# Optimization experiments

Measured on AMD Instinct MI355X. Metric: run time of the kernel, lower is better.

The kernel has to match this reference:

```python
import jax, jax.numpy as jnp
import numpy as np

EPS = 1e-5
B, CIN, COUT, H, W, RED = 2, 64, 128, 256, 256, 8
K = 9  # 3x3 deformable kernel taps


def conv2d(x, w, b=None, pad=0):
    out = jax.lax.conv_general_dilated(x, w, (1, 1), [(pad, pad), (pad, pad)],
                                       dimension_numbers=('NCHW', 'OIHW', 'NCHW'))
    return out if b is None else out + b[None, :, None, None]


def batchnorm(x, g, b, m, v):
    s = g / jnp.sqrt(v + EPS)
    return x * s[None, :, None, None] + (b - m * s)[None, :, None, None]


def bilinear_sample(x, py, px):
    # x:(B,C,H,W), py/px:(B,K,H,W) float coords -> (B,C,K,H,W); zero outside bounds
    Bx, C, Hx, Wx = x.shape
    y0 = jnp.floor(py); x0 = jnp.floor(px)
    flat = x.reshape(Bx, C, Hx * Wx)

    def gather(yi, xi):
        valid = (yi >= 0) & (yi < Hx) & (xi >= 0) & (xi < Wx)
        idx = jnp.clip(yi, 0, Hx - 1) * Wx + jnp.clip(xi, 0, Wx - 1)
        g = jax.vmap(lambda f, i: jnp.take(f, i, axis=1))(flat, idx.reshape(Bx, -1))
        return g.reshape(Bx, C, *yi.shape[1:]) * valid[:, None].astype(x.dtype)

    wy1 = (py - y0)[:, None]; wy0 = 1.0 - wy1
    wx1 = (px - x0)[:, None]; wx0 = 1.0 - wx1
    y0i = y0.astype(jnp.int32); x0i = x0.astype(jnp.int32)
    return (gather(y0i, x0i) * wy0 * wx0 + gather(y0i, x0i + 1) * wy0 * wx1 +
            gather(y0i + 1, x0i) * wy1 * wx0 + gather(y0i + 1, x0i + 1) * wy1 * wx1)


def deform_conv(x, offsets, w, b):
    # torchvision DeformConv2d v1: offsets (B, 2*K, H, W), (dy,dx) per tap, row-major taps
    Bx, Cin, Hx, Wx = x.shape
    off = offsets.reshape(Bx, K, 2, Hx, Wx)
    ky, kx = jnp.meshgrid(jnp.arange(3), jnp.arange(3), indexing='ij')
    base_y = (jnp.arange(Hx)[None, :, None] + (ky.reshape(K) - 1)[:, None, None]).astype(x.dtype)  # (K,H,1)
    base_x = (jnp.arange(Wx)[None, None, :] + (kx.reshape(K) - 1)[:, None, None]).astype(x.dtype)  # (K,1,W)
    py = base_y[None] + off[:, :, 0]  # (B,K,H,W)
    px = base_x[None] + off[:, :, 1]
    sampled = bilinear_sample(x, py, px)  # (B,Cin,K,H,W)
    out = jnp.einsum('bckhw,ock->bohw', sampled, w.reshape(w.shape[0], Cin, K))
    return out + b[None, :, None, None]


def setup_inputs() -> dict:
    key = jax.random.key(0)
    ks = jax.random.split(key, 20)
    r = lambda i, shape, s=1.0: jax.random.normal(ks[i], shape, jnp.float32) * s
    cr = COUT // RED
    return dict(
        x=r(0, (B, CIN, H, W)),
        w_off=r(1, (2 * K, CIN, 3, 3), 0.04), b_off=jnp.zeros((2 * K,), jnp.float32),
        w_def=r(2, (COUT, CIN, 3, 3), 0.04), b_def=r(3, (COUT,), 0.01),
        bn_gamma=jnp.ones((COUT,), jnp.float32) + r(4, (COUT,), 0.1),
        bn_beta=r(5, (COUT,), 0.1),
        bn_mean=r(6, (COUT,), 0.1),
        bn_var=jax.random.uniform(ks[7], (COUT,), jnp.float32, 0.5, 1.5),
        se_w=r(8, (cr, COUT, 1, 1), 0.1), se_b=r(9, (cr,), 0.01),
        se_bn_gamma=jnp.ones((cr,), jnp.float32) + r(10, (cr,), 0.1),
        se_bn_beta=r(11, (cr,), 0.1),
        se_bn_mean=r(12, (cr,), 0.1),
        se_bn_var=jax.random.uniform(ks[13], (cr,), jnp.float32, 0.5, 1.5),
        phi=r(14, (cr, COUT), 0.3),
        ds_w=r(15, (COUT, CIN, 1, 1), 0.1),
        ds_bn_gamma=jnp.ones((COUT,), jnp.float32) + r(16, (COUT,), 0.1),
        ds_bn_beta=r(17, (COUT,), 0.1),
        ds_bn_mean=r(18, (COUT,), 0.1),
        ds_bn_var=jax.random.uniform(ks[19], (COUT,), jnp.float32, 0.5, 1.5),
    )


def reference(x, w_off, b_off, w_def, b_def, bn_gamma, bn_beta, bn_mean, bn_var,
              se_w, se_b, se_bn_gamma, se_bn_beta, se_bn_mean, se_bn_var, phi,
              ds_w, ds_bn_gamma, ds_bn_beta, ds_bn_mean, ds_bn_var):
    offsets = conv2d(x, w_off, b_off, pad=1)
    out = deform_conv(x, offsets, w_def, b_def)
    out = batchnorm(out, bn_gamma, bn_beta, bn_mean, bn_var)
    # DCSE: global-avg-pool -> 1x1 conv -> BN -> GELU -> matmul with softmax(phi) -> sigmoid gate
    pooled = out.mean(axis=(2, 3))  # (B,COUT)
    t = pooled @ se_w[:, :, 0, 0].T + se_b  # (B,COUT//RED)
    s = se_bn_gamma / jnp.sqrt(se_bn_var + EPS)
    t = jax.nn.gelu(t * s[None] + (se_bn_beta - se_bn_mean * s)[None], approximate=False)
    dw = jax.nn.sigmoid(t @ jax.nn.softmax(phi, axis=-1))  # (B,COUT)
    out = out * dw[:, :, None, None]
    identity = batchnorm(conv2d(x, ds_w), ds_bn_gamma, ds_bn_beta, ds_bn_mean, ds_bn_var)
    return jax.nn.relu(out + identity)
```

## Files before the change

### kernel.cpp

```cpp
#include <hip/hip_runtime.h>
#include <hip/hip_bf16.h>

typedef __hip_bfloat16 bf16;
typedef unsigned int u32;
typedef __attribute__((ext_vector_type(8))) short bf16x8;
typedef __attribute__((ext_vector_type(4))) float f32x4;

#define HHW 65536
#define SBH 584
#define SWU 292
#define REDW 132

__device__ __forceinline__ float b2f(bf16 v) { return __bfloat162float(v); }
__device__ __forceinline__ bf16  f2b(float v) { return __float2bfloat16(v); }
__device__ __forceinline__ float blo(u32 p) { return __uint_as_float(p << 16); }
__device__ __forceinline__ float bhi(u32 p) { return __uint_as_float(p & 0xffff0000u); }
__device__ __forceinline__ u32 pack2(float lo, float hi) {
    bf16 a = f2b(lo), c = f2b(hi);
    unsigned short ua, uc;
    __builtin_memcpy(&ua, &a, 2); __builtin_memcpy(&uc, &c, 2);
    return (u32)ua | ((u32)uc << 16);
}

__global__ __launch_bounds__(256) void k_prep(const float* __restrict__ x, bf16* __restrict__ xT,
        const float* __restrict__ w_off, const float* __restrict__ w_def, const float* __restrict__ b_def,
        const float* __restrict__ bng, const float* __restrict__ bnb, const float* __restrict__ bnm, const float* __restrict__ bnv,
        const float* __restrict__ ds_w, const float* __restrict__ dsg, const float* __restrict__ dsb,
        const float* __restrict__ dsm, const float* __restrict__ dsv,
        bf16* __restrict__ Wf, float* __restrict__ wloff, float* __restrict__ dws2,
        float* __restrict__ bnS, float* __restrict__ bnT2, float* __restrict__ dsT) {
    __shared__ bf16 tile[64][66];
    int g = blockIdx.x;
    int t = threadIdx.x;
    if (g < 2048) {
        int b = g >> 10;
        int pixbase = (g & 1023) << 6;
        int pix = t & 63, ci0 = t >> 6;
        const float* xb = x + ((size_t)b * 64) * HHW + pixbase + pix;
        for (int ci = ci0; ci < 64; ci += 4)
            tile[pix][ci] = f2b(xb[(size_t)ci * HHW]);
        __syncthreads();
        bf16* dst = xT + ((size_t)b * HHW + pixbase) * 64;
        for (int i = t; i < 4096; i += 256)
            dst[i] = tile[i >> 6][i & 63];
        return;
    }
    int tid = (g - 2048) * 256 + t;
    for (int i = tid; i < 8 * 18 * 64 * 8; i += 8192) {
        int j = i & 7, lane = (i >> 3) & 63;
        int rem = i >> 9;
        int ks = rem % 18, ct = rem / 18;
        int co = ct * 16 + (lane & 15);
        int K  = ks * 32 + ((lane >> 4) << 3) + j;
        int ci = K & 63, kk = K >> 6;
        Wf[i] = f2b(w_def[co * 576 + ci * 9 + kk]);
    }
    for (int i = tid; i < 576 * 20; i += 8192) {
        int kci = i / 20, j = i - kci * 20;
        wloff[i] = (j < 18) ? w_off[j * 576 + kci] : 0.f;
    }
    if (tid < 8192) {
        int co = tid >> 6;
        float s2 = dsg[co] * rsqrtf(dsv[co] + 1e-5f);
        dws2[tid] = ds_w[tid] * s2;
    }
    if (tid < 128) {
        float s = bng[tid] * rsqrtf(bnv[tid] + 1e-5f);
        bnS[tid] = s;
        bnT2[tid] = (b_def[tid] - bnm[tid]) * s + bnb[tid];
        float s2 = dsg[tid] * rsqrtf(dsv[tid] + 1e-5f);
        dsT[tid] = dsb[tid] - dsm[tid] * s2;
    }
}

__global__ __launch_bounds__(256) void k_off(const float* __restrict__ x,
        const float* __restrict__ wloff, const float* __restrict__ b_off,
        uint4* __restrict__ orec, float4* __restrict__ wrec) {
    int g = blockIdx.x;
    int b = g >> 8, h = g & 255;
    int t = threadIdx.x;
    float acc[20];
    #pragma unroll
    for (int j = 0; j < 20; ++j) acc[j] = 0.f;
    const float* xb = x + ((size_t)b * 64) * HHW;
    for (int ci = 0; ci < 64; ++ci) {
        const float* xc = xb + (size_t)ci * HHW;
        #pragma unroll
        for (int ky = 0; ky < 3; ++ky) {
            int y = h + ky - 1;
            if ((unsigned)y >= 256u) continue;
            const float* row = xc + y * 256;
            float v0 = (t >= 1)   ? row[t - 1] : 0.f;
            float v1 = row[t];
            float v2 = (t <= 254) ? row[t + 1] : 0.f;
            const float4* wr = (const float4*)(wloff + (ci * 9 + ky * 3) * 20);
            #pragma unroll
            for (int q = 0; q < 5; ++q) {
                float4 wv = wr[q];
                acc[q*4+0] += v0 * wv.x; acc[q*4+1] += v0 * wv.y;
                acc[q*4+2] += v0 * wv.z; acc[q*4+3] += v0 * wv.w;
            }
            #pragma unroll
            for (int q = 0; q < 5; ++q) {
                float4 wv = wr[5 + q];
                acc[q*4+0] += v1 * wv.x; acc[q*4+1] += v1 * wv.y;
                acc[q*4+2] += v1 * wv.z; acc[q*4+3] += v1 * wv.w;
            }
            #pragma unroll
            for (int q = 0; q < 5; ++q) {
                float4 wv = wr[10 + q];
                acc[q*4+0] += v2 * wv.x; acc[q*4+1] += v2 * wv.y;
                acc[q*4+2] += v2 * wv.z; acc[q*4+3] += v2 * wv.w;
            }
        }
    }
    int tile = (h << 2) + (t >> 6);
    int pix  = t & 63;
    size_t rbase = ((size_t)(b * 1024 + tile)) * 576;
    #pragma unroll
    for (int k = 0; k < 9; ++k) {
        int ky = k / 3, kx = k - ky * 3;
        float dy = acc[2 * k]     + b_off[2 * k];
        float dx = acc[2 * k + 1] + b_off[2 * k + 1];
        float py = (float)(h + ky - 1) + dy;
        float px = (float)(t + kx - 1) + dx;
        float fy = floorf(py), fx = floorf(px);
        int y0 = (int)fy, x0 = (int)fx;
        float wy1 = py - fy, wx1 = px - fx;
        float wy0 = 1.f - wy1, wx0 = 1.f - wx1;
        int y1 = y0 + 1, x1 = x0 + 1;
        int yc0 = min(max(y0, 0), 255), yc1 = min(max(y1, 0), 255);
        int xc0 = min(max(x0, 0), 255), xc1 = min(max(x1, 0), 255);
        float m0 = ((unsigned)y0 < 256u) ? 1.f : 0.f;
        float m1 = ((unsigned)y1 < 256u) ? 1.f : 0.f;
        float n0 = ((unsigned)x0 < 256u) ? 1.f : 0.f;
        float n1 = ((unsigned)x1 < 256u) ? 1.f : 0.f;
        uint4 o;
        o.x = ((u32)(yc0 * 256 + xc0)) << 5;
        o.y = ((u32)(yc0 * 256 + xc1)) << 5;
        o.z = ((u32)(yc1 * 256 + xc0)) << 5;
        o.w = ((u32)(yc1 * 256 + xc1)) << 5;
        float4 wv;
        wv.x = wy0 * wx0 * m0 * n0;
        wv.y = wy0 * wx1 * m0 * n1;
        wv.z = wy1 * wx0 * m1 * n0;
        wv.w = wy1 * wx1 * m1 * n1;
        orec[rbase + k * 64 + pix] = o;
        wrec[rbase + k * 64 + pix] = wv;
    }
}

__global__ __launch_bounds__(256) void k_deform(const bf16* __restrict__ xT,
        const uint4* __restrict__ orec, const float4* __restrict__ wrec,
        const bf16* __restrict__ Wf,
        const float* __restrict__ bnS, const float* __restrict__ bnT2,
        bf16* __restrict__ out_pre, float* __restrict__ part) {
    __shared__ bf16 smem[64 * SBH];
    int blk = blockIdx.x;
    int b = blk >> 10;
    int tile = blk & 1023;
    int pixbase = tile << 6;
    int t = threadIdx.x;
    int wid = t >> 6, l = t & 63;

    {
        int cig = l & 31, hf = l >> 5;
        size_t rbase = ((size_t)(b * 1024 + tile)) * 576;
        const uint4*  orc = orec + rbase;
        const float4* wrc = wrec + rbase;
        const u32* xw = (const u32*)xT + (size_t)b * (HHW * 32);
        u32* sw = (u32*)smem;
        #pragma unroll 4
        for (int it = 0; it < 72; ++it) {
            int r = (it << 3) + (wid << 1) + hf;
            uint4  o  = orc[r];
            float4 wv = wrc[r];
            u32 p00 = xw[o.x + cig];
            u32 p01 = xw[o.y + cig];
            u32 p10 = xw[o.z + cig];
            u32 p11 = xw[o.w + cig];
            float lo = blo(p00)*wv.x + blo(p01)*wv.y + blo(p10)*wv.z + blo(p11)*wv.w;
            float hi = bhi(p00)*wv.x + bhi(p01)*wv.y + bhi(p10)*wv.z + bhi(p11)*wv.w;
            int k9 = r >> 6, pix = r & 63;
            sw[pix * SWU + (k9 << 5) + cig] = pack2(lo, hi);
        }
    }
    __syncthreads();

    int wp = wid << 4;
    int lr = l & 15, lg = l >> 4;
    f32x4 acc[8];
    #pragma unroll
    for (int ct = 0; ct < 8; ++ct) acc[ct] = (f32x4){0.f, 0.f, 0.f, 0.f};
    const bf16* arow = smem + (wp + lr) * SBH + lg * 8;
    const bf16* wbase = Wf + l * 8;
    #pragma unroll
    for (int ks = 0; ks < 18; ++ks) {
        bf16x8 af = *(const bf16x8*)(arow + ks * 32);
        #pragma unroll
        for (int ct = 0; ct < 8; ++ct) {
            bf16x8 bfr = *(const bf16x8*)(wbase + (ct * 18 + ks) * 512);
            acc[ct] = __builtin_amdgcn_mfma_f32_16x16x32_bf16(af, bfr, acc[ct], 0, 0, 0);
        }
    }
    __syncthreads();
    float* red = (float*)smem;
    #pragma unroll
    for (int ct = 0; ct < 8; ++ct) {
        int co = ct * 16 + lr;
        float sc = bnS[co], sh = bnT2[co];
        #pragma unroll
        for (int r = 0; r < 4; ++r) {
            int m = lg * 4 + r;
            red[(wp + m) * REDW + co] = acc[ct][r] * sc + sh;
        }
    }
    __syncthreads();
    bf16* op = out_pre + ((size_t)b * HHW + pixbase) * 128;
    for (int i = t; i < 8192; i += 256)
        op[i] = f2b(red[(i >> 7) * REDW + (i & 127)]);
    if (t < 128) {
        float sum = 0.f;
        #pragma unroll
        for (int p = 0; p < 64; ++p) sum += red[p * REDW + t];
        part[((size_t)(b * 128 + t)) * 1024 + tile] = sum;
    }
}

__global__ __launch_bounds__(256) void k_pool(const float* __restrict__ part, float* __restrict__ pooled) {
    int bco = blockIdx.x;
    int t = threadIdx.x;
    const float* p = part + (size_t)bco * 1024;
    float sum = 0.f;
    for (int i = t; i < 1024; i += 256) sum += p[i];
    __shared__ float r[256];
    r[t] = sum; __syncthreads();
    for (int ofs = 128; ofs > 0; ofs >>= 1) {
        if (t < ofs) r[t] += r[t + ofs];
        __syncthreads();
    }
    if (t == 0) pooled[bco] = r[0] * (1.f / 65536.f);
}

__global__ __launch_bounds__(256) void k_se(const float* __restrict__ pooled,
        const float* __restrict__ se_w, const float* __restrict__ se_b,
        const float* __restrict__ sg_, const float* __restrict__ sb_,
        const float* __restrict__ sm_, const float* __restrict__ sv_,
        const float* __restrict__ phi, float* __restrict__ dw) {
    __shared__ float tl[32];
    __shared__ float sp[16][128];
    __shared__ float pl[256];
    int t = threadIdx.x;
    pl[t] = pooled[t];
    __syncthreads();
    if (t < 32) {
        int b = t >> 4, r = t & 15;
        float d = se_b[r];
        for (int c = 0; c < 128; ++c) d += pl[b * 128 + c] * se_w[r * 128 + c];
        float s = sg_[r] * rsqrtf(sv_[r] + 1e-5f);
        float xb = d * s + (sb_[r] - sm_[r] * s);
        tl[t] = 0.5f * xb * (1.f + erff(xb * 0.70710678118654752f));
    }
    if (t >= 32 && t < 48) {
        int r = t - 32;
        float m = -1e30f;
        for (int c = 0; c < 128; ++c) m = fmaxf(m, phi[r * 128 + c]);
        float ssum = 0.f;
        for (int c = 0; c < 128; ++c) { float e = expf(phi[r * 128 + c] - m); sp[r][c] = e; ssum += e; }
        float inv = 1.f / ssum;
        for (int c = 0; c < 128; ++c) sp[r][c] *= inv;
    }
    __syncthreads();
    {
        int b = t >> 7, co = t & 127;
        float a = 0.f;
        #pragma unroll
        for (int r = 0; r < 16; ++r) a += tl[b * 16 + r] * sp[r][co];
        dw[t] = 1.f / (1.f + expf(-a));
    }
}

__global__ __launch_bounds__(256) void k_final(const bf16* __restrict__ xT,
        const bf16* __restrict__ out_pre, const float* __restrict__ dws2,
        const float* __restrict__ dsT, const float* __restrict__ dw,
        float* __restrict__ out) {
    __shared__ float xtile[64 * 68];
    __shared__ float otile[64 * 129];
    __shared__ float dwl[128], dsTl[128];
    int g = blockIdx.x;
    int b = g >> 10;
    int pixbase = (g & 1023) << 6;
    int t = threadIdx.x;
    const bf16* xp = xT + ((size_t)b * HHW + pixbase) * 64;
    for (int i = t; i < 4096; i += 256)
        xtile[(i >> 6) * 68 + (i & 63)] = b2f(xp[i]);
    if (t < 128) { dwl[t] = dw[b * 128 + t]; dsTl[t] = dsT[t]; }
    __syncthreads();
    int co = t >> 1, half = t & 1;
    float4 wr[16];
    const float4* wp = (const float4*)(dws2 + co * 64);
    #pragma unroll
    for (int i = 0; i < 16; ++i) wr[i] = wp[i];
    float dwv = dwl[co], dst = dsTl[co];
    const bf16* opp = out_pre + ((size_t)b * HHW + pixbase) * 128 + co;
    for (int p0 = 0; p0 < 32; ++p0) {
        int p = half * 32 + p0;
        const float* xr = xtile + p * 68;
        float a = 0.f;
        #pragma unroll
        for (int i = 0; i < 16; ++i) {
            float4 xv = *(const float4*)(xr + i * 4);
            a += xv.x * wr[i].x + xv.y * wr[i].y + xv.z * wr[i].z + xv.w * wr[i].w;
        }
        float opre = b2f(opp[(size_t)p * 128]);
        float v = opre * dwv + a + dst;
        otile[p * 129 + co] = fmaxf(v, 0.f);
    }
    __syncthreads();
    float* ob = out + (size_t)b * 128 * HHW + pixbase;
    for (int i = t; i < 8192; i += 256) {
        int cco = i >> 6, pp = i & 63;
        ob[(size_t)cco * HHW + pp] = otile[pp * 129 + cco];
    }
}

extern "C" void kernel_launch(void* const* d_in, const int* in_sizes, int n_in,
                              void* d_out, int out_size, void* d_ws, size_t ws_size,
                              hipStream_t stream) {
    const float* x     = (const float*)d_in[0];
    const float* w_off = (const float*)d_in[1];
    const float* b_off = (const float*)d_in[2];
    const float* w_def = (const float*)d_in[3];
    const float* b_def = (const float*)d_in[4];
    const float* bng   = (const float*)d_in[5];
    const float* bnb   = (const float*)d_in[6];
    const float* bnm   = (const float*)d_in[7];
    const float* bnv   = (const float*)d_in[8];
    const float* se_w  = (const float*)d_in[9];
    const float* se_b  = (const float*)d_in[10];
    const float* sbg   = (const float*)d_in[11];
    const float* sbb   = (const float*)d_in[12];
    const float* sbm   = (const float*)d_in[13];
    const float* sbv   = (const float*)d_in[14];
    const float* phi   = (const float*)d_in[15];
    const float* ds_w  = (const float*)d_in[16];
    const float* dsg   = (const float*)d_in[17];
    const float* dsb   = (const float*)d_in[18];
    const float* dsm   = (const float*)d_in[19];
    const float* dsv   = (const float*)d_in[20];
    float* out = (float*)d_out;

    char* w = (char*)d_ws;
    bf16*  xT     = (bf16*)w;   w += 16777216;
    bf16*  Wf     = (bf16*)w;   w += 147456;
    float* wloff  = (float*)w;  w += 46080;
    float* dws2   = (float*)w;  w += 32768;
    float* bnS    = (float*)w;  w += 512;
    float* bnT2   = (float*)w;  w += 512;
    float* dsT    = (float*)w;  w += 512;
    bf16*  opre   = (bf16*)w;   w += 33554432;
    float* part   = (float*)w;  w += 1048576;
    float* pooled = (float*)w;  w += 1024;
    float* dwv    = (float*)w;  w += 1024;
    uint4*  orec  = (uint4*)w;  w += 18874368;
    float4* wrec  = (float4*)w; w += 18874368;

    hipLaunchKernelGGL(k_prep, dim3(2080), dim3(256), 0, stream, x, xT, w_off, w_def, b_def,
                       bng, bnb, bnm, bnv, ds_w, dsg, dsb, dsm, dsv,
                       Wf, wloff, dws2, bnS, bnT2, dsT);
    hipLaunchKernelGGL(k_off, dim3(512), dim3(256), 0, stream, x, wloff, b_off, orec, wrec);
    hipLaunchKernelGGL(k_deform, dim3(2048), dim3(256), 0, stream, xT, orec, wrec, Wf, bnS, bnT2, opre, part);
    hipLaunchKernelGGL(k_pool, dim3(256), dim3(256), 0, stream, part, pooled);
    hipLaunchKernelGGL(k_se, dim3(1), dim3(256), 0, stream, pooled, se_w, se_b, sbg, sbb, sbm, sbv, phi, dwv);
    hipLaunchKernelGGL(k_final, dim3(2048), dim3(256), 0, stream, xT, opre, dws2, dsT, dwv, out);
}
```

Measured before the change: 442.7 us.

## Compress bilinear sample records, widen deform blocks, swizzle tiles, vectorize transpose store

Bilinear sampling records shrink from two 16-byte structs per tap to a packed 4-byte coordinate word plus four bf16 weights, which cuts the write and read traffic between the offset and deform kernels. The deform kernel moves to 512 threads, with each pair of waves splitting the output channels, software-prefetches the next record in the gather loop, and swizzles block indices across batches and tiles. The transpose in the prep kernel stores 32-bit words instead of single bf16 values. Rounding the bilinear weights to bf16 adds some numerical error, and the wider block uses more registers per CU.

```diff
diff --git a/kernel.cpp b/kernel.cpp
--- a/kernel.cpp
+++ b/kernel.cpp
@@ -40,9 +40,12 @@
         for (int ci = ci0; ci < 64; ci += 4)
             tile[pix][ci] = f2b(xb[(size_t)ci * HHW]);
         __syncthreads();
-        bf16* dst = xT + ((size_t)b * HHW + pixbase) * 64;
-        for (int i = t; i < 4096; i += 256)
-            dst[i] = tile[i >> 6][i & 63];
+        u32* dst32 = (u32*)(xT + ((size_t)b * HHW + pixbase) * 64);
+        const u32* t32 = (const u32*)&tile[0][0];
+        for (int i = t; i < 2048; i += 256) {
+            int pix2 = i >> 5, j = i & 31;
+            dst32[i] = t32[pix2 * 33 + j];
+        }
         return;
     }
     int tid = (g - 2048) * 256 + t;
@@ -75,7 +78,7 @@
 
 __global__ __launch_bounds__(256) void k_off(const float* __restrict__ x,
         const float* __restrict__ wloff, const float* __restrict__ b_off,
-        uint4* __restrict__ orec, float4* __restrict__ wrec) {
+        u32* __restrict__ crec, uint2* __restrict__ wrec) {
     int g = blockIdx.x;
     int b = g >> 8, h = g & 255;
     int t = threadIdx.x;
@@ -129,36 +132,31 @@
         float wy1 = py - fy, wx1 = px - fx;
         float wy0 = 1.f - wy1, wx0 = 1.f - wx1;
         int y1 = y0 + 1, x1 = x0 + 1;
-        int yc0 = min(max(y0, 0), 255), yc1 = min(max(y1, 0), 255);
-        int xc0 = min(max(x0, 0), 255), xc1 = min(max(x1, 0), 255);
+        u32 yc0 = (u32)min(max(y0, 0), 255), yc1 = (u32)min(max(y1, 0), 255);
+        u32 xc0 = (u32)min(max(x0, 0), 255), xc1 = (u32)min(max(x1, 0), 255);
         float m0 = ((unsigned)y0 < 256u) ? 1.f : 0.f;
         float m1 = ((unsigned)y1 < 256u) ? 1.f : 0.f;
         float n0 = ((unsigned)x0 < 256u) ? 1.f : 0.f;
         float n1 = ((unsigned)x1 < 256u) ? 1.f : 0.f;
-        uint4 o;
-        o.x = ((u32)(yc0 * 256 + xc0)) << 5;
-        o.y = ((u32)(yc0 * 256 + xc1)) << 5;
-        o.z = ((u32)(yc1 * 256 + xc0)) << 5;
-        o.w = ((u32)(yc1 * 256 + xc1)) << 5;
-        float4 wv;
-        wv.x = wy0 * wx0 * m0 * n0;
-        wv.y = wy0 * wx1 * m0 * n1;
-        wv.z = wy1 * wx0 * m1 * n0;
-        wv.w = wy1 * wx1 * m1 * n1;
-        orec[rbase + k * 64 + pix] = o;
+        u32 c = yc0 | (xc0 << 8) | (yc1 << 16) | (xc1 << 24);
+        uint2 wv;
+        wv.x = pack2(wy0 * wx0 * m0 * n0, wy0 * wx1 * m0 * n1);
+        wv.y = pack2(wy1 * wx0 * m1 * n0, wy1 * wx1 * m1 * n1);
+        crec[rbase + k * 64 + pix] = c;
         wrec[rbase + k * 64 + pix] = wv;
     }
 }
 
-__global__ __launch_bounds__(256) void k_deform(const bf16* __restrict__ xT,
-        const uint4* __restrict__ orec, const float4* __restrict__ wrec,
+__global__ __launch_bounds__(512, 4) void k_deform(const bf16* __restrict__ xT,
+        const u32* __restrict__ crec, const uint2* __restrict__ wrec,
         const bf16* __restrict__ Wf,
         const float* __restrict__ bnS, const float* __restrict__ bnT2,
         bf16* __restrict__ out_pre, float* __restrict__ part) {
     __shared__ bf16 smem[64 * SBH];
     int blk = blockIdx.x;
-    int b = blk >> 10;
-    int tile = blk & 1023;
+    int swz = (blk & 7) * 256 + (blk >> 3);
+    int b = swz >> 10;
+    int tile = swz & 1023;
     int pixbase = tile << 6;
     int t = threadIdx.x;
     int wid = t >> 6, l = t & 63;
@@ -166,48 +164,56 @@
     {
         int cig = l & 31, hf = l >> 5;
         size_t rbase = ((size_t)(b * 1024 + tile)) * 576;
-        const uint4*  orc = orec + rbase;
-        const float4* wrc = wrec + rbase;
+        const u32*  crc = crec + rbase;
+        const uint2* wrc = wrec + rbase;
         const u32* xw = (const u32*)xT + (size_t)b * (HHW * 32);
         u32* sw = (u32*)smem;
-        #pragma unroll 4
-        for (int it = 0; it < 72; ++it) {
-            int r = (it << 3) + (wid << 1) + hf;
-            uint4  o  = orc[r];
-            float4 wv = wrc[r];
-            u32 p00 = xw[o.x + cig];
-            u32 p01 = xw[o.y + cig];
-            u32 p10 = xw[o.z + cig];
-            u32 p11 = xw[o.w + cig];
-            float lo = blo(p00)*wv.x + blo(p01)*wv.y + blo(p10)*wv.z + blo(p11)*wv.w;
-            float hi = bhi(p00)*wv.x + bhi(p01)*wv.y + bhi(p10)*wv.z + bhi(p11)*wv.w;
+        int r = (wid << 1) + hf;
+        u32  c0 = crc[r];
+        uint2 w0 = wrc[r];
+        #pragma unroll 6
+        for (int it = 0; it < 36; ++it) {
+            u32 c = c0; uint2 wv = w0;
+            c0 = crc[r + 16]; w0 = wrc[r + 16];
+            u32 y0 = c & 255u, x0 = (c >> 8) & 255u, y1 = (c >> 16) & 255u, x1 = c >> 24;
+            u32 o00 = (y0 << 13) + (x0 << 5) + cig;
+            u32 o01 = (y0 << 13) + (x1 << 5) + cig;
+            u32 o10 = (y1 << 13) + (x0 << 5) + cig;
+            u32 o11 = (y1 << 13) + (x1 << 5) + cig;
+            u32 p00 = xw[o00], p01 = xw[o01], p10 = xw[o10], p11 = xw[o11];
+            float w00 = blo(wv.x), w01 = bhi(wv.x), w10 = blo(wv.y), w11 = bhi(wv.y);
+            float lo = blo(p00)*w00 + blo(p01)*w01 + blo(p10)*w10 + blo(p11)*w11;
+            float hi = bhi(p00)*w00 + bhi(p01)*w01 + bhi(p10)*w10 + bhi(p11)*w11;
             int k9 = r >> 6, pix = r & 63;
             sw[pix * SWU + (k9 << 5) + cig] = pack2(lo, hi);
-        }
-    }
-    __syncthreads();
-
-    int wp = wid << 4;
+            r += 16;
+        }
+    }
+    __syncthreads();
+
+    int pxg = wid >> 1, coh = wid & 1;
+    int wp = pxg << 4;
     int lr = l & 15, lg = l >> 4;
-    f32x4 acc[8];
-    #pragma unroll
-    for (int ct = 0; ct < 8; ++ct) acc[ct] = (f32x4){0.f, 0.f, 0.f, 0.f};
+    f32x4 acc[4];
+    #pragma unroll
+    for (int ct = 0; ct < 4; ++ct) acc[ct] = (f32x4){0.f, 0.f, 0.f, 0.f};
     const bf16* arow = smem + (wp + lr) * SBH + lg * 8;
     const bf16* wbase = Wf + l * 8;
     #pragma unroll
     for (int ks = 0; ks < 18; ++ks) {
         bf16x8 af = *(const bf16x8*)(arow + ks * 32);
         #pragma unroll
-        for (int ct = 0; ct < 8; ++ct) {
-            bf16x8 bfr = *(const bf16x8*)(wbase + (ct * 18 + ks) * 512);
+        for (int ct = 0; ct < 4; ++ct) {
+            int cti = coh * 4 + ct;
+            bf16x8 bfr = *(const bf16x8*)(wbase + (cti * 18 + ks) * 512);
             acc[ct] = __builtin_amdgcn_mfma_f32_16x16x32_bf16(af, bfr, acc[ct], 0, 0, 0);
         }
     }
     __syncthreads();
     float* red = (float*)smem;
     #pragma unroll
-    for (int ct = 0; ct < 8; ++ct) {
-        int co = ct * 16 + lr;
+    for (int ct = 0; ct < 4; ++ct) {
+        int co = (coh * 4 + ct) * 16 + lr;
         float sc = bnS[co], sh = bnT2[co];
         #pragma unroll
         for (int r = 0; r < 4; ++r) {
@@ -217,7 +223,7 @@
     }
     __syncthreads();
     bf16* op = out_pre + ((size_t)b * HHW + pixbase) * 128;
-    for (int i = t; i < 8192; i += 256)
+    for (int i = t; i < 8192; i += 512)
         op[i] = f2b(red[(i >> 7) * REDW + (i & 127)]);
     if (t < 128) {
         float sum = 0.f;
@@ -362,14 +368,14 @@
     float* part   = (float*)w;  w += 1048576;
     float* pooled = (float*)w;  w += 1024;
     float* dwv    = (float*)w;  w += 1024;
-    uint4*  orec  = (uint4*)w;  w += 18874368;
-    float4* wrec  = (float4*)w; w += 18874368;
+    u32*   crec   = (u32*)w;    w += 4720896;
+    uint2* wrec   = (uint2*)w;  w += 9441792;
 
     hipLaunchKernelGGL(k_prep, dim3(2080), dim3(256), 0, stream, x, xT, w_off, w_def, b_def,
                        bng, bnb, bnm, bnv, ds_w, dsg, dsb, dsm, dsv,
                        Wf, wloff, dws2, bnS, bnT2, dsT);
-    hipLaunchKernelGGL(k_off, dim3(512), dim3(256), 0, stream, x, wloff, b_off, orec, wrec);
-    hipLaunchKernelGGL(k_deform, dim3(2048), dim3(256), 0, stream, xT, orec, wrec, Wf, bnS, bnT2, opre, part);
+    hipLaunchKernelGGL(k_off, dim3(512), dim3(256), 0, stream, x, wloff, b_off, crec, wrec);
+    hipLaunchKernelGGL(k_deform, dim3(2048), dim3(512), 0, stream, xT, crec, wrec, Wf, bnS, bnT2, opre, part);
     hipLaunchKernelGGL(k_pool, dim3(256), dim3(256), 0, stream, part, pooled);
     hipLaunchKernelGGL(k_se, dim3(1), dim3(256), 0, stream, pooled, se_w, se_b, sbg, sbb, sbm, sbv, phi, dwv);
     hipLaunchKernelGGL(k_final, dim3(2048), dim3(256), 0, stream, xT, opre, dws2, dsT, dwv, out);
```

Result: faster. 422.5 us (-4.6%).
